# Kernel tuning notes

Measured on AMD Instinct MI355X. Metric: run time of the kernel, lower is better.

## Reference

```python
import jax, jax.numpy as jnp
import numpy as np

B, S, D = 64, 4096, 256
LN_EPS = 1e-3  # Keras LayerNormalization default epsilon


def setup_inputs() -> dict:
    key = jax.random.key(0)
    k1, k2, k3 = jax.random.split(key, 3)
    x = jax.random.normal(k1, (B, S, D), dtype=jnp.float32)
    mask = jnp.ones((B, S), dtype=jnp.float32)
    gamma = jnp.ones((D,), dtype=jnp.float32)       # LayerNorm scale
    beta = jnp.zeros((D,), dtype=jnp.float32)       # LayerNorm offset
    w = jax.random.normal(k2, (D,), dtype=jnp.float32) * (1.0 / np.sqrt(D))  # Dense(1) kernel
    b = jnp.zeros((), dtype=jnp.float32)            # Dense(1) bias
    return {"x": x, "mask": mask, "gamma": gamma, "beta": beta, "w": w, "b": b}


def reference(x, mask, gamma, beta, w, b):
    # LayerNorm over feature dim
    mu = jnp.mean(x, axis=-1, keepdims=True)
    var = jnp.mean(jnp.square(x - mu), axis=-1, keepdims=True)
    xn = (x - mu) * jax.lax.rsqrt(var + LN_EPS) * gamma + beta  # [B,S,D]
    # Dense(1) score projection
    score = jnp.einsum('bsd,d->bs', xn, w) + b                  # [B,S]
    # Mask out padded positions, softmax over sequence axis
    score = score + (1.0 - mask) * -1e9
    weights = jax.nn.softmax(score, axis=1)                     # [B,S]
    # Weighted sum over sequence
    return jnp.einsum('bsd,bs->bd', x, weights)                 # [B,D]
```

## Files before the change

### kernel.cpp

```cpp
#include <hip/hip_runtime.h>
#include <math.h>

#define B_   64
#define S_   4096
#define D_   256
#define CH   32
#define ROWS_PER_CHUNK (S_ / CH)
#define WAVES_PER_BLOCK 4
#define ROWS_PER_WAVE (ROWS_PER_CHUNK / WAVES_PER_BLOCK)
#define LN_EPS 1e-3f

__global__ __launch_bounds__(256) void pool_pass1(
    const float* __restrict__ x, const float* __restrict__ mask,
    const float* __restrict__ gamma, const float* __restrict__ w,
    float* __restrict__ ws_acc, float* __restrict__ ws_m, float* __restrict__ ws_l)
{
    const int blk   = blockIdx.x;
    const int b     = blk / CH;
    const int chunk = blk % CH;
    const int tid   = threadIdx.x;
    const int lane  = tid & 63;
    const int wave  = tid >> 6;
    const int d0    = lane * 4;

    const float4 g4 = *(const float4*)(gamma + d0);
    const float4 w4 = *(const float4*)(w + d0);
    float4 gw;
    gw.x = g4.x * w4.x; gw.y = g4.y * w4.y; gw.z = g4.z * w4.z; gw.w = g4.w * w4.w;
    float sgw = gw.x + gw.y + gw.z + gw.w;
    #pragma unroll
    for (int off = 32; off > 0; off >>= 1) sgw += __shfl_xor(sgw, off, 64);

    const int row0 = chunk * ROWS_PER_CHUNK + wave;
    const float* xrow = x + ((size_t)b * S_ + row0) * D_ + d0;
    const float* mrow = mask + (size_t)b * S_ + row0;

    float  m = -3.0e38f;
    float  l = 0.0f;
    float4 acc = make_float4(0.f, 0.f, 0.f, 0.f);

    float4 v   = *(const float4*)(xrow);
    float  msk = mrow[0];

    #pragma unroll 4
    for (int r = 0; r < ROWS_PER_WAVE; ++r) {
        const int rn = (r + 1 < ROWS_PER_WAVE) ? (r + 1) : r;
        float4 vnext = *(const float4*)(xrow + (size_t)rn * WAVES_PER_BLOCK * D_);
        float  mnext = mrow[rn * WAVES_PER_BLOCK];

        float s1 = v.x + v.y + v.z + v.w;
        float s2 = v.x*v.x + v.y*v.y + v.z*v.z + v.w*v.w;
        float s3 = v.x*gw.x + v.y*gw.y + v.z*gw.z + v.w*gw.w;
        #pragma unroll
        for (int off = 32; off > 0; off >>= 1) {
            s1 += __shfl_xor(s1, off, 64);
            s2 += __shfl_xor(s2, off, 64);
            s3 += __shfl_xor(s3, off, 64);
        }
        const float mu    = s1 * (1.0f / D_);
        const float var   = s2 * (1.0f / D_) - mu * mu;
        const float rstd  = rsqrtf(var + LN_EPS);
        const float score = rstd * (s3 - mu * sgw) + (1.0f - msk) * -1e9f;

        const float mn    = fmaxf(m, score);
        const float scale = __expf(m - mn);
        const float p     = __expf(score - mn);
        m = mn;
        l = l * scale + p;
        acc.x = acc.x * scale + p * v.x;
        acc.y = acc.y * scale + p * v.y;
        acc.z = acc.z * scale + p * v.z;
        acc.w = acc.w * scale + p * v.w;

        v = vnext; msk = mnext;
    }

    __shared__ float s_acc[WAVES_PER_BLOCK][D_];
    __shared__ float s_m[WAVES_PER_BLOCK];
    __shared__ float s_l[WAVES_PER_BLOCK];
    *(float4*)&s_acc[wave][d0] = acc;
    if (lane == 0) { s_m[wave] = m; s_l[wave] = l; }
    __syncthreads();

    const float M  = fmaxf(fmaxf(s_m[0], s_m[1]), fmaxf(s_m[2], s_m[3]));
    const float e0 = __expf(s_m[0] - M), e1 = __expf(s_m[1] - M);
    const float e2 = __expf(s_m[2] - M), e3 = __expf(s_m[3] - M);
    const float L  = e0 * s_l[0] + e1 * s_l[1] + e2 * s_l[2] + e3 * s_l[3];
    const float a  = e0 * s_acc[0][tid] + e1 * s_acc[1][tid]
                   + e2 * s_acc[2][tid] + e3 * s_acc[3][tid];

    ws_acc[(size_t)blk * D_ + tid] = a;
    if (tid == 0) { ws_m[blk] = M; ws_l[blk] = L; }
}

__global__ __launch_bounds__(256) void pool_pass2(
    const float* __restrict__ ws_acc, const float* __restrict__ ws_m,
    const float* __restrict__ ws_l, float* __restrict__ out)
{
    const int b = blockIdx.x;
    const int d = threadIdx.x;

    float M = -3.0e38f;
    #pragma unroll
    for (int c = 0; c < CH; ++c) M = fmaxf(M, ws_m[b * CH + c]);

    float L = 0.0f, a = 0.0f;
    #pragma unroll
    for (int c = 0; c < CH; ++c) {
        const float e = __expf(ws_m[b * CH + c] - M);
        L += e * ws_l[b * CH + c];
        a += e * ws_acc[((size_t)(b * CH + c)) * D_ + d];
    }
    out[(size_t)b * D_ + d] = a / L;
}

extern "C" void kernel_launch(void* const* d_in, const int* in_sizes, int n_in,
                              void* d_out, int out_size, void* d_ws, size_t ws_size,
                              hipStream_t stream) {
    const float* x     = (const float*)d_in[0];
    const float* mask  = (const float*)d_in[1];
    const float* gamma = (const float*)d_in[2];
    const float* w     = (const float*)d_in[4];
    float* out = (float*)d_out;

    float* ws_acc = (float*)d_ws;
    float* ws_m   = ws_acc + (size_t)B_ * CH * D_;
    float* ws_l   = ws_m + B_ * CH;

    pool_pass1<<<B_ * CH, 256, 0, stream>>>(x, mask, gamma, w, ws_acc, ws_m, ws_l);
    pool_pass2<<<B_, 256, 0, stream>>>(ws_acc, ws_m, ws_l, out);
}
```

Measured before the change: 373.3 us.

## Process four rows per wave with 16-lane row groups to shorten reductions

Each wave is split into four 16-lane groups, and each group owns one row, with every lane holding 16 features across four float4 loads. This cuts the cross-lane shuffle reduction from 6 steps to 4 per row and gives more independent memory loads in flight per thread. The cost is higher register use and a 16-way shared-memory merge of the per-group online-softmax states at block end instead of 4-way.

Result: faster. 363.0 us (-2.7%).

```diff
diff --git a/kernel.cpp b/kernel.cpp
--- a/kernel.cpp
+++ b/kernel.cpp
@@ -6,8 +6,9 @@
 #define D_   256
 #define CH   32
 #define ROWS_PER_CHUNK (S_ / CH)
-#define WAVES_PER_BLOCK 4
-#define ROWS_PER_WAVE (ROWS_PER_CHUNK / WAVES_PER_BLOCK)
+#define NWAVE 4
+#define ROWS_PER_BLOCK_ITER (NWAVE * 4)
+#define NITER (ROWS_PER_CHUNK / ROWS_PER_BLOCK_ITER)
 #define LN_EPS 1e-3f
 
 __global__ __launch_bounds__(256) void pool_pass1(
@@ -21,38 +22,55 @@
     const int tid   = threadIdx.x;
     const int lane  = tid & 63;
     const int wave  = tid >> 6;
-    const int d0    = lane * 4;
+    const int q     = lane >> 4;
+    const int t     = lane & 15;
 
-    const float4 g4 = *(const float4*)(gamma + d0);
-    const float4 w4 = *(const float4*)(w + d0);
-    float4 gw;
-    gw.x = g4.x * w4.x; gw.y = g4.y * w4.y; gw.z = g4.z * w4.z; gw.w = g4.w * w4.w;
-    float sgw = gw.x + gw.y + gw.z + gw.w;
+    float4 gw[4];
+    float sgw = 0.0f;
     #pragma unroll
-    for (int off = 32; off > 0; off >>= 1) sgw += __shfl_xor(sgw, off, 64);
+    for (int k = 0; k < 4; ++k) {
+        const int d = t * 4 + 64 * k;
+        const float4 g4 = *(const float4*)(gamma + d);
+        const float4 w4 = *(const float4*)(w + d);
+        gw[k].x = g4.x * w4.x; gw[k].y = g4.y * w4.y;
+        gw[k].z = g4.z * w4.z; gw[k].w = g4.w * w4.w;
+        sgw += gw[k].x + gw[k].y + gw[k].z + gw[k].w;
+    }
+    #pragma unroll
+    for (int off = 8; off > 0; off >>= 1) sgw += __shfl_xor(sgw, off, 64);
 
-    const int row0 = chunk * ROWS_PER_CHUNK + wave;
-    const float* xrow = x + ((size_t)b * S_ + row0) * D_ + d0;
-    const float* mrow = mask + (size_t)b * S_ + row0;
+    const int row0 = chunk * ROWS_PER_CHUNK + wave * 4 + q;
+    const float* xbase = x + ((size_t)b * S_ + row0) * D_ + t * 4;
+    const float* mbase = mask + (size_t)b * S_ + row0;
 
     float  m = -3.0e38f;
     float  l = 0.0f;
-    float4 acc = make_float4(0.f, 0.f, 0.f, 0.f);
+    float4 acc[4];
+    #pragma unroll
+    for (int k = 0; k < 4; ++k) acc[k] = make_float4(0.f, 0.f, 0.f, 0.f);
 
-    float4 v   = *(const float4*)(xrow);
-    float  msk = mrow[0];
+    float4 v[4];
+    #pragma unroll
+    for (int k = 0; k < 4; ++k) v[k] = *(const float4*)(xbase + 64 * k);
+    float msk = mbase[0];
 
-    #pragma unroll 4
-    for (int r = 0; r < ROWS_PER_WAVE; ++r) {
-        const int rn = (r + 1 < ROWS_PER_WAVE) ? (r + 1) : r;
-        float4 vnext = *(const float4*)(xrow + (size_t)rn * WAVES_PER_BLOCK * D_);
-        float  mnext = mrow[rn * WAVES_PER_BLOCK];
+    for (int i = 0; i < NITER; ++i) {
+        const int inx = (i + 1 < NITER) ? i + 1 : i;
+        float4 vn[4];
+        #pragma unroll
+        for (int k = 0; k < 4; ++k)
+            vn[k] = *(const float4*)(xbase + (size_t)inx * ROWS_PER_BLOCK_ITER * D_ + 64 * k);
+        const float mskn = mbase[inx * ROWS_PER_BLOCK_ITER];
 
-        float s1 = v.x + v.y + v.z + v.w;
-        float s2 = v.x*v.x + v.y*v.y + v.z*v.z + v.w*v.w;
-        float s3 = v.x*gw.x + v.y*gw.y + v.z*gw.z + v.w*gw.w;
+        float s1 = 0.f, s2 = 0.f, s3 = 0.f;
         #pragma unroll
-        for (int off = 32; off > 0; off >>= 1) {
+        for (int k = 0; k < 4; ++k) {
+            s1 += v[k].x + v[k].y + v[k].z + v[k].w;
+            s2 += v[k].x*v[k].x + v[k].y*v[k].y + v[k].z*v[k].z + v[k].w*v[k].w;
+            s3 += v[k].x*gw[k].x + v[k].y*gw[k].y + v[k].z*gw[k].z + v[k].w*gw[k].w;
+        }
+        #pragma unroll
+        for (int off = 8; off > 0; off >>= 1) {
             s1 += __shfl_xor(s1, off, 64);
             s2 += __shfl_xor(s2, off, 64);
             s3 += __shfl_xor(s3, off, 64);
@@ -62,33 +80,43 @@
         const float rstd  = rsqrtf(var + LN_EPS);
         const float score = rstd * (s3 - mu * sgw) + (1.0f - msk) * -1e9f;
 
-        const float mn    = fmaxf(m, score);
-        const float scale = __expf(m - mn);
-        const float p     = __expf(score - mn);
-        m = mn;
+        const float mnew  = fmaxf(m, score);
+        const float scale = __expf(m - mnew);
+        const float p     = __expf(score - mnew);
+        m = mnew;
         l = l * scale + p;
-        acc.x = acc.x * scale + p * v.x;
-        acc.y = acc.y * scale + p * v.y;
-        acc.z = acc.z * scale + p * v.z;
-        acc.w = acc.w * scale + p * v.w;
+        #pragma unroll
+        for (int k = 0; k < 4; ++k) {
+            acc[k].x = acc[k].x * scale + p * v[k].x;
+            acc[k].y = acc[k].y * scale + p * v[k].y;
+            acc[k].z = acc[k].z * scale + p * v[k].z;
+            acc[k].w = acc[k].w * scale + p * v[k].w;
+        }
 
-        v = vnext; msk = mnext;
+        #pragma unroll
+        for (int k = 0; k < 4; ++k) v[k] = vn[k];
+        msk = mskn;
     }
 
-    __shared__ float s_acc[WAVES_PER_BLOCK][D_];
-    __shared__ float s_m[WAVES_PER_BLOCK];
-    __shared__ float s_l[WAVES_PER_BLOCK];
-    *(float4*)&s_acc[wave][d0] = acc;
-    if (lane == 0) { s_m[wave] = m; s_l[wave] = l; }
+    __shared__ float s_acc[NWAVE * 4][D_];
+    __shared__ float s_m[NWAVE * 4];
+    __shared__ float s_l[NWAVE * 4];
+    const int g = wave * 4 + q;
+    #pragma unroll
+    for (int k = 0; k < 4; ++k) *(float4*)&s_acc[g][t * 4 + 64 * k] = acc[k];
+    if (t == 0) { s_m[g] = m; s_l[g] = l; }
     __syncthreads();
 
-    const float M  = fmaxf(fmaxf(s_m[0], s_m[1]), fmaxf(s_m[2], s_m[3]));
-    const float e0 = __expf(s_m[0] - M), e1 = __expf(s_m[1] - M);
-    const float e2 = __expf(s_m[2] - M), e3 = __expf(s_m[3] - M);
-    const float L  = e0 * s_l[0] + e1 * s_l[1] + e2 * s_l[2] + e3 * s_l[3];
-    const float a  = e0 * s_acc[0][tid] + e1 * s_acc[1][tid]
-                   + e2 * s_acc[2][tid] + e3 * s_acc[3][tid];
-
+    float M = -3.0e38f;
+    #pragma unroll
+    for (int gg = 0; gg < 16; ++gg) M = fmaxf(M, s_m[gg]);
+    float L = 0.f, a = 0.f;
+    #pragma unroll
+    for (int gg = 0; gg < 16; ++gg) {
+        const float e = __expf(s_m[gg] - M);
+        L += e * s_l[gg];
+        a += e * s_acc[gg][tid];
+    }
     ws_acc[(size_t)blk * D_ + tid] = a;
     if (tid == 0) { ws_m[blk] = M; ws_l[blk] = L; }
 }
```
